# Kernel tuning notes

Measured on AMD Instinct MI355X. Metric: run time of the kernel, lower is better.

Reference implementation:

```python
import jax, jax.numpy as jnp
import numpy as np

EPS = 1e-07
B, C, NCON, NCC = 500000, 30, 8, 3
NH = 7  # hidden width


def _coarse_code():
    # [C, NCC] Gaussian bump coarse code, as built in __init__
    sigma = 0.25
    const_1 = 1.0 / (sigma * np.sqrt(6.28))
    ii = jnp.arange(C, dtype=jnp.float32)[:, None] / (C - 1)
    jj = jnp.arange(NCC, dtype=jnp.float32)[None, :] / (NCC - 1)
    return (const_1 * jnp.exp(-0.5 * jnp.square((ii - jj) / sigma))).astype(jnp.float32)


def _mlp(x, W1, b1, Wh, bh, Wo, bo):
    # x: [B, C, n_in]; six 7-unit ReLU layers then linear output (dropout inactive)
    h = jax.nn.relu(jnp.einsum('bci,hi->bch', x, W1) + b1)
    for i in range(Wh.shape[0]):
        h = jax.nn.relu(jnp.einsum('bci,hi->bch', h, Wh[i]) + bh[i])
    return jnp.einsum('bci,oi->bco', h, Wo) + bo


def setup_inputs() -> dict:
    key = jax.random.key(0)
    ks = jax.random.split(key, 16)
    u = lambda k, shape, lo, hi: jax.random.uniform(k, shape, jnp.float32, lo, hi)
    inp = {
        'tau': jax.random.uniform(ks[0], (B, C, NCON), jnp.float32),
        'mu_direct': jax.random.uniform(ks[1], (B, 1), jnp.float32),
        'mu_diffuse': jax.random.uniform(ks[2], (B, 1), jnp.float32),
        # net_direct: n_input = 5 + NCC + 1 = 9
        'Wd1': u(ks[3], (NH, 5 + NCC + 1), -1.0, 1.0),
        'bd1': u(ks[4], (NH,), 0.9, 1.1),
        'Wdh': u(ks[5], (5, NH, NH), -1.0, 1.0),
        'bdh': u(ks[6], (5, NH), 0.9, 1.1),
        'Wdo': u(ks[7], (3, NH), -1.0, 1.0),
        'bdo': u(ks[8], (3,), -0.1, 0.1),
        # net_diffuse: n_input = 5 + NCC = 8
        'Wf1': u(ks[9], (NH, 5 + NCC), -1.0, 1.0),
        'bf1': u(ks[10], (NH,), 0.9, 1.1),
        'Wfh': u(ks[11], (5, NH, NH), -1.0, 1.0),
        'bfh': u(ks[12], (5, NH), 0.9, 1.1),
        'Wfo': u(ks[13], (3, NH), -1.0, 1.0),
        'bfo': u(ks[14], (3,), -0.1, 0.1),
    }
    return inp


def reference(tau, mu_direct, mu_diffuse, Wd1, bd1, Wdh, bdh, Wdo, bdo,
              Wf1, bf1, Wfh, bfh, Wfo, bfo):
    tau_total = jnp.sum(tau, axis=2)                      # [B, C]
    t_direct = jnp.exp(-tau_total / (mu_direct + EPS))    # [B, C]
    t_diffuse = jnp.exp(-tau_total / (mu_diffuse + EPS))  # [B, C]

    mu_d = mu_direct[:, :, None]                          # [B, 1, 1]
    tau_direct = tau / (mu_d + EPS)                       # [B, C, NCON]

    direct_1 = (tau_direct[:, :, 3] + tau_direct[:, :, 4]
                + tau_direct[:, :, 6] + tau_direct[:, :, 7])[:, :, None]
    mu_rep = jnp.broadcast_to(mu_d, (tau.shape[0], C, 1))
    cc = jnp.broadcast_to(_coarse_code()[None], (tau.shape[0], C, NCC))

    direct = jnp.concatenate([tau_direct[:, :, 0:2], tau_direct[:, :, 5:6],
                              tau_direct[:, :, 2:3], direct_1, mu_rep, cc], axis=2)  # [B,C,9]

    diffuse_1 = (tau[:, :, 3] + tau[:, :, 4] + tau[:, :, 6] + tau[:, :, 7])[:, :, None]
    diffuse = jnp.concatenate([tau[:, :, 0:2], tau[:, :, 5:6],
                               tau[:, :, 2:3], diffuse_1, cc], axis=2)  # [B,C,8]

    e_split_direct = jax.nn.softmax(_mlp(direct, Wd1, bd1, Wdh, bdh, Wdo, bdo), axis=-1)
    e_split_diffuse = jax.nn.softmax(_mlp(diffuse, Wf1, bf1, Wfh, bfh, Wfo, bfo), axis=-1)
    return (t_direct, t_diffuse, e_split_direct, e_split_diffuse)
```

## Files before the change

### kernel.cpp

```cpp
#include <hip/hip_runtime.h>


#define B_SZ 500000
#define C_SZ 30
#define BC   (B_SZ * C_SZ)
#define EPSF 1e-7f

__device__ __forceinline__ float bf2f(unsigned short u) {
    union { unsigned int i; float f; } v;
    v.i = ((unsigned int)u) << 16;
    return v.f;
}

__device__ __forceinline__ unsigned short f2bf(float f) {
    union { float f; unsigned int i; } v;
    v.f = f;
    unsigned int u = v.i;
    unsigned int r = u + 0x7fffu + ((u >> 16) & 1u);
    return (unsigned short)(r >> 16);
}

__global__ void detect_dtype(const unsigned int* __restrict__ tau_raw,
                             int* __restrict__ flag) {
    if (threadIdx.x == 0 && blockIdx.x == 0) {
        unsigned int acc = 0;
        for (int i = 0; i < 256; ++i) acc |= tau_raw[i];
        *flag = (acc & 0x8000u) ? 1 : 0;
    }
}

struct P12 { const void* p[12]; };

__global__ void cvt_weights(P12 ptrs, float* __restrict__ ws,
                            const int* __restrict__ flag) {
    int i = blockIdx.x * blockDim.x + threadIdx.x;
    if (i >= 741) return;
    const int sizes[12] = {63, 7, 245, 35, 21, 3, 56, 7, 245, 35, 21, 3};
    int off = i, seg = 0;
    while (seg < 11 && off >= sizes[seg]) { off -= sizes[seg]; ++seg; }
    if (*flag) {
        ws[i] = ((const float*)ptrs.p[seg])[off];
    } else {
        ws[i] = bf2f(((const unsigned short*)ptrs.p[seg])[off]);
    }
}

template <int IN>
__device__ __forceinline__ void mlp(const float* __restrict__ x,
                                    const float* __restrict__ W1,
                                    const float* __restrict__ b1,
                                    const float* __restrict__ Wh,
                                    const float* __restrict__ bh,
                                    const float* __restrict__ Wo,
                                    const float* __restrict__ bo,
                                    float* __restrict__ o) {
    float h[7];
#pragma unroll
    for (int j = 0; j < 7; ++j) {
        float a = b1[j];
#pragma unroll
        for (int i = 0; i < IN; ++i) a = fmaf(x[i], W1[j * IN + i], a);
        h[j] = fmaxf(a, 0.0f);
    }
#pragma unroll
    for (int l = 0; l < 5; ++l) {
        float h2[7];
#pragma unroll
        for (int j = 0; j < 7; ++j) {
            float a = bh[l * 7 + j];
#pragma unroll
            for (int i = 0; i < 7; ++i) a = fmaf(h[i], Wh[l * 49 + j * 7 + i], a);
            h2[j] = fmaxf(a, 0.0f);
        }
#pragma unroll
        for (int j = 0; j < 7; ++j) h[j] = h2[j];
    }
#pragma unroll
    for (int k = 0; k < 3; ++k) {
        float a = bo[k];
#pragma unroll
        for (int i = 0; i < 7; ++i) a = fmaf(h[i], Wo[k * 7 + i], a);
        o[k] = a;
    }
}

__global__ __launch_bounds__(256) void scatter_main(
    const void* __restrict__ tau_p,
    const void* __restrict__ mu_dir_p,
    const void* __restrict__ mu_dif_p,
    const float* __restrict__ ws,
    const int* __restrict__ flag,
    void* __restrict__ out_p)
{
    __shared__ float cc_s[C_SZ * 3];
    int tid = threadIdx.x;
    if (tid < C_SZ * 3) {
        int c = tid / 3, j = tid - c * 3;
        const float sigma = 0.25f;
        const float c1 = 1.0f / (sigma * sqrtf(6.28f));
        float ii = (float)c * (1.0f / (float)(C_SZ - 1));
        float jj = (float)j * 0.5f;
        float d = (ii - jj) * (1.0f / sigma);
        cc_s[tid] = c1 * __expf(-0.5f * d * d);
    }
    __syncthreads();

    int e = blockIdx.x * 256 + tid;
    if (e >= BC) return;
    int b = e / C_SZ;
    int c = e - b * C_SZ;

    int is_f32 = *flag;

    float t0, t1, t2, t3, t4, t5, t6, t7, mu_d, mu_f;
    if (is_f32) {
        const float4* tf = (const float4*)tau_p;
        float4 a = tf[2 * e];
        float4 bq = tf[2 * e + 1];
        t0 = a.x; t1 = a.y; t2 = a.z; t3 = a.w;
        t4 = bq.x; t5 = bq.y; t6 = bq.z; t7 = bq.w;
        mu_d = ((const float*)mu_dir_p)[b];
        mu_f = ((const float*)mu_dif_p)[b];
    } else {
        uint4 t = ((const uint4*)tau_p)[e];
        t0 = bf2f((unsigned short)(t.x & 0xffffu));
        t1 = bf2f((unsigned short)(t.x >> 16));
        t2 = bf2f((unsigned short)(t.y & 0xffffu));
        t3 = bf2f((unsigned short)(t.y >> 16));
        t4 = bf2f((unsigned short)(t.z & 0xffffu));
        t5 = bf2f((unsigned short)(t.z >> 16));
        t6 = bf2f((unsigned short)(t.w & 0xffffu));
        t7 = bf2f((unsigned short)(t.w >> 16));
        mu_d = bf2f(((const unsigned short*)mu_dir_p)[b]);
        mu_f = bf2f(((const unsigned short*)mu_dif_p)[b]);
    }

    float rcp_d = __builtin_amdgcn_rcpf(mu_d + EPSF);
    float rcp_f = __builtin_amdgcn_rcpf(mu_f + EPSF);

    float tau_total = ((t0 + t1) + (t2 + t3)) + ((t4 + t5) + (t6 + t7));
    float t_direct = __expf(-tau_total * rcp_d);
    float t_diffuse = __expf(-tau_total * rcp_f);

    float cc0 = cc_s[c * 3 + 0], cc1 = cc_s[c * 3 + 1], cc2 = cc_s[c * 3 + 2];
    float s1 = (t3 + t4) + (t6 + t7);

    float xd[9] = {t0 * rcp_d, t1 * rcp_d, t5 * rcp_d, t2 * rcp_d,
                   s1 * rcp_d, mu_d, cc0, cc1, cc2};
    float xf[8] = {t0, t1, t5, t2, s1, cc0, cc1, cc2};

    float od[3], of_[3];
    mlp<9>(xd, ws + 0, ws + 63, ws + 70, ws + 315, ws + 350, ws + 371, od);
    mlp<8>(xf, ws + 374, ws + 430, ws + 437, ws + 682, ws + 717, ws + 738, of_);

    float md = fmaxf(fmaxf(od[0], od[1]), od[2]);
    float d0 = __expf(od[0] - md), d1 = __expf(od[1] - md), d2 = __expf(od[2] - md);
    float rd = __builtin_amdgcn_rcpf(d0 + d1 + d2);
    float mf = fmaxf(fmaxf(of_[0], of_[1]), of_[2]);
    float f0 = __expf(of_[0] - mf), f1 = __expf(of_[1] - mf), f2 = __expf(of_[2] - mf);
    float rf = __builtin_amdgcn_rcpf(f0 + f1 + f2);

    int od_base = 2 * BC + 3 * e;
    int of_base = 5 * BC + 3 * e;
    if (is_f32) {
        float* out = (float*)out_p;
        out[e] = t_direct;
        out[BC + e] = t_diffuse;
        out[od_base + 0] = d0 * rd;
        out[od_base + 1] = d1 * rd;
        out[od_base + 2] = d2 * rd;
        out[of_base + 0] = f0 * rf;
        out[of_base + 1] = f1 * rf;
        out[of_base + 2] = f2 * rf;
    } else {
        unsigned short* out = (unsigned short*)out_p;
        out[e] = f2bf(t_direct);
        out[BC + e] = f2bf(t_diffuse);
        out[od_base + 0] = f2bf(d0 * rd);
        out[od_base + 1] = f2bf(d1 * rd);
        out[od_base + 2] = f2bf(d2 * rd);
        out[of_base + 0] = f2bf(f0 * rf);
        out[of_base + 1] = f2bf(f1 * rf);
        out[of_base + 2] = f2bf(f2 * rf);
    }
}

extern "C" void kernel_launch(void* const* d_in, const int* in_sizes, int n_in,
                              void* d_out, int out_size, void* d_ws, size_t ws_size,
                              hipStream_t stream) {
    float* ws = (float*)d_ws;
    int* flag = (int*)((char*)d_ws + 4096);

    detect_dtype<<<1, 64, 0, stream>>>((const unsigned int*)d_in[0], flag);

    P12 p;
    for (int i = 0; i < 12; ++i) p.p[i] = d_in[3 + i];
    cvt_weights<<<1, 768, 0, stream>>>(p, ws, flag);

    int nblk = (BC + 255) / 256;
    scatter_main<<<nblk, 256, 0, stream>>>(
        d_in[0], d_in[1], d_in[2], ws, flag, d_out);
}
```

Baseline: 919.3 us.

## Fold coarse-code into per-channel biases, use fdot2 for diffuse MLP, merge prep kernels

Folds the constant coarse-code inputs into per-channel effective first-layer biases, so the first layer of each MLP gets narrower. It also remaps the diffuse MLP's first layer onto the raw tau columns and runs the diffuse MLP with packed fp16 dot products (fdot2) on the bf16 path. Other changes: exp2 with LOG2E folded into the weights, packed bf16 conversion for stores, and dtype detection merged into a single prep kernel. The fp16 hidden activations lower precision and may affect accuracy.

```diff
diff --git a/kernel.cpp b/kernel.cpp
--- a/kernel.cpp
+++ b/kernel.cpp
@@ -5,6 +5,35 @@
 #define C_SZ 30
 #define BC   (B_SZ * C_SZ)
 #define EPSF 1e-7f
+#define LOG2E 1.4426950408889634f
+
+#if __has_builtin(__builtin_amdgcn_fdot2)
+#define HAVE_FDOT2 1
+#else
+#define HAVE_FDOT2 0
+#endif
+
+typedef __fp16 h2 __attribute__((ext_vector_type(2)));
+
+enum {
+    WD1C  = 0,
+    WDH   = 42,
+    BDH   = 287,
+    WDO   = 322,
+    BDO   = 343,
+    BEFFD = 352,
+    BEFFF = 592,
+    VF16  = 832,
+    WFH16 = 860,
+    WFO16 = 1000,
+    BFO   = 1012,
+    BFH   = 1015,
+    VFF   = 1056,
+    WFHF  = 1112,
+    WFOF  = 1357,
+    WS_FLOATS = 1378
+};
+#define FLAG_BYTE_OFF 6144
 
 __device__ __forceinline__ float bf2f(unsigned short u) {
     union { unsigned int i; float f; } v;
@@ -12,76 +41,104 @@
     return v.f;
 }
 
-__device__ __forceinline__ unsigned short f2bf(float f) {
-    union { float f; unsigned int i; } v;
-    v.f = f;
-    unsigned int u = v.i;
-    unsigned int r = u + 0x7fffu + ((u >> 16) & 1u);
-    return (unsigned short)(r >> 16);
-}
-
-__global__ void detect_dtype(const unsigned int* __restrict__ tau_raw,
-                             int* __restrict__ flag) {
-    if (threadIdx.x == 0 && blockIdx.x == 0) {
-        unsigned int acc = 0;
-        for (int i = 0; i < 256; ++i) acc |= tau_raw[i];
-        *flag = (acc & 0x8000u) ? 1 : 0;
-    }
-}
+__device__ __forceinline__ float ex2(float x) {
+    float r;
+    asm("v_exp_f32 %0, %1" : "=v"(r) : "v"(x));
+    return r;
+}
+
+__device__ __forceinline__ unsigned int pk_bf16(float lo, float hi) {
+    unsigned int r;
+    asm("v_cvt_pk_bf16_f32 %0, %1, %2" : "=v"(r) : "v"(lo), "v"(hi));
+    return r;
+}
+
+#if HAVE_FDOT2
+__device__ __forceinline__ h2 uash2(unsigned int u) {
+    union { unsigned int u; h2 h; } v; v.u = u; return v.h;
+}
+#endif
 
 struct P12 { const void* p[12]; };
 
-__global__ void cvt_weights(P12 ptrs, float* __restrict__ ws,
-                            const int* __restrict__ flag) {
-    int i = blockIdx.x * blockDim.x + threadIdx.x;
-    if (i >= 741) return;
-    const int sizes[12] = {63, 7, 245, 35, 21, 3, 56, 7, 245, 35, 21, 3};
-    int off = i, seg = 0;
-    while (seg < 11 && off >= sizes[seg]) { off -= sizes[seg]; ++seg; }
-    if (*flag) {
-        ws[i] = ((const float*)ptrs.p[seg])[off];
-    } else {
-        ws[i] = bf2f(((const unsigned short*)ptrs.p[seg])[off]);
-    }
-}
-
-template <int IN>
-__device__ __forceinline__ void mlp(const float* __restrict__ x,
-                                    const float* __restrict__ W1,
-                                    const float* __restrict__ b1,
-                                    const float* __restrict__ Wh,
-                                    const float* __restrict__ bh,
-                                    const float* __restrict__ Wo,
-                                    const float* __restrict__ bo,
-                                    float* __restrict__ o) {
-    float h[7];
-#pragma unroll
-    for (int j = 0; j < 7; ++j) {
-        float a = b1[j];
-#pragma unroll
-        for (int i = 0; i < IN; ++i) a = fmaf(x[i], W1[j * IN + i], a);
-        h[j] = fmaxf(a, 0.0f);
-    }
-#pragma unroll
-    for (int l = 0; l < 5; ++l) {
-        float h2[7];
-#pragma unroll
-        for (int j = 0; j < 7; ++j) {
-            float a = bh[l * 7 + j];
-#pragma unroll
-            for (int i = 0; i < 7; ++i) a = fmaf(h[i], Wh[l * 49 + j * 7 + i], a);
-            h2[j] = fmaxf(a, 0.0f);
-        }
-#pragma unroll
-        for (int j = 0; j < 7; ++j) h[j] = h2[j];
-    }
-#pragma unroll
-    for (int k = 0; k < 3; ++k) {
-        float a = bo[k];
-#pragma unroll
-        for (int i = 0; i < 7; ++i) a = fmaf(h[i], Wo[k * 7 + i], a);
-        o[k] = a;
-    }
+__global__ void prep(P12 ptrs, const unsigned int* __restrict__ tau_raw,
+                     float* __restrict__ ws, int* __restrict__ flagp)
+{
+    __shared__ int sflag;
+    int tid = threadIdx.x;
+    if (tid < 64) {
+        unsigned long long m = __ballot((tau_raw[tid] & 0x8000u) != 0u);
+        if (tid == 0) { sflag = (m != 0ull) ? 1 : 0; *flagp = sflag; }
+    }
+    __syncthreads();
+    const int f32m = sflag;
+
+    auto rd = [&](int seg, int idx) -> float {
+        if (f32m) return ((const float*)ptrs.p[seg])[idx];
+        return bf2f(((const unsigned short*)ptrs.p[seg])[idx]);
+    };
+    auto ccf = [&](int c, int k) -> float {
+        const float C1 = 1.0f / (0.25f * sqrtf(6.28f));
+        float ii = (float)c * (1.0f / 29.0f);
+        float jj = (float)k * 0.5f;
+        float d = (ii - jj) * 4.0f;
+        return C1 * expf(-0.5f * d * d);
+    };
+    auto pk = [&](float a, float b) -> unsigned int {
+        union { h2 h; unsigned int u; } v;
+        v.h.x = (__fp16)a; v.h.y = (__fp16)b;
+        return v.u;
+    };
+    unsigned int* wsu = (unsigned int*)ws;
+
+    for (int i = tid; i < 42; i += 256) { int j = i / 6, k = i % 6; ws[WD1C + i] = rd(0, j * 9 + k); }
+    for (int i = tid; i < 245; i += 256) ws[WDH + i] = rd(2, i);
+    for (int i = tid; i < 35;  i += 256) ws[BDH + i] = rd(3, i);
+    for (int i = tid; i < 21;  i += 256) ws[WDO + i] = rd(4, i) * LOG2E;
+    for (int i = tid; i < 3;   i += 256) ws[BDO + i] = rd(5, i) * LOG2E;
+    for (int i = tid; i < 240; i += 256) {
+        int c = i / 8, j = i % 8; float v = 0.f;
+        if (j < 7) v = rd(1, j) + rd(0, j * 9 + 6) * ccf(c, 0)
+                               + rd(0, j * 9 + 7) * ccf(c, 1)
+                               + rd(0, j * 9 + 8) * ccf(c, 2);
+        ws[BEFFD + i] = v;
+    }
+    for (int i = tid; i < 240; i += 256) {
+        int c = i / 8, j = i % 8; float v = 0.f;
+        if (j < 7) v = rd(7, j) + rd(6, j * 8 + 5) * ccf(c, 0)
+                               + rd(6, j * 8 + 6) * ccf(c, 1)
+                               + rd(6, j * 8 + 7) * ccf(c, 2);
+        ws[BEFFF + i] = v;
+    }
+    for (int i = tid; i < 28; i += 256) {
+        int j = i / 4, p = i % 4; float lo, hi;
+        if      (p == 0) { lo = rd(6, j * 8 + 0); hi = rd(6, j * 8 + 1); }
+        else if (p == 1) { lo = rd(6, j * 8 + 3); hi = rd(6, j * 8 + 4); }
+        else if (p == 2) { lo = rd(6, j * 8 + 4); hi = rd(6, j * 8 + 2); }
+        else             { lo = rd(6, j * 8 + 4); hi = rd(6, j * 8 + 4); }
+        wsu[VF16 + i] = pk(lo, hi);
+    }
+    for (int i = tid; i < 140; i += 256) {
+        int lj = i / 4, p = i % 4; float lo, hi;
+        if (p < 3) { lo = rd(8, lj * 7 + 2 * p); hi = rd(8, lj * 7 + 2 * p + 1); }
+        else       { lo = rd(8, lj * 7 + 6);     hi = 0.f; }
+        wsu[WFH16 + i] = pk(lo, hi);
+    }
+    for (int i = tid; i < 12; i += 256) {
+        int j = i / 4, p = i % 4; float lo, hi;
+        if (p < 3) { lo = rd(10, j * 7 + 2 * p); hi = rd(10, j * 7 + 2 * p + 1); }
+        else       { lo = rd(10, j * 7 + 6);     hi = 0.f; }
+        wsu[WFO16 + i] = pk(lo, hi);
+    }
+    for (int i = tid; i < 3;   i += 256) ws[BFO + i] = rd(11, i);
+    for (int i = tid; i < 35;  i += 256) ws[BFH + i] = rd(9, i);
+    for (int i = tid; i < 56; i += 256) {
+        int j = i / 8, k = i % 8;
+        const int cols[8] = {0, 1, 3, 4, 4, 2, 4, 4};
+        ws[VFF + i] = rd(6, j * 8 + cols[k]);
+    }
+    for (int i = tid; i < 245; i += 256) ws[WFHF + i] = rd(8, i);
+    for (int i = tid; i < 21;  i += 256) ws[WFOF + i] = rd(10, i);
 }
 
 __global__ __launch_bounds__(256) void scatter_main(
@@ -92,20 +149,7 @@
     const int* __restrict__ flag,
     void* __restrict__ out_p)
 {
-    __shared__ float cc_s[C_SZ * 3];
-    int tid = threadIdx.x;
-    if (tid < C_SZ * 3) {
-        int c = tid / 3, j = tid - c * 3;
-        const float sigma = 0.25f;
-        const float c1 = 1.0f / (sigma * sqrtf(6.28f));
-        float ii = (float)c * (1.0f / (float)(C_SZ - 1));
-        float jj = (float)j * 0.5f;
-        float d = (ii - jj) * (1.0f / sigma);
-        cc_s[tid] = c1 * __expf(-0.5f * d * d);
-    }
-    __syncthreads();
-
-    int e = blockIdx.x * 256 + tid;
+    int e = blockIdx.x * 256 + threadIdx.x;
     if (e >= BC) return;
     int b = e / C_SZ;
     int c = e - b * C_SZ;
@@ -139,49 +183,170 @@
     float rcp_f = __builtin_amdgcn_rcpf(mu_f + EPSF);
 
     float tau_total = ((t0 + t1) + (t2 + t3)) + ((t4 + t5) + (t6 + t7));
-    float t_direct = __expf(-tau_total * rcp_d);
-    float t_diffuse = __expf(-tau_total * rcp_f);
-
-    float cc0 = cc_s[c * 3 + 0], cc1 = cc_s[c * 3 + 1], cc2 = cc_s[c * 3 + 2];
+    float ttl = tau_total * LOG2E;
+    float t_direct  = ex2(-ttl * rcp_d);
+    float t_diffuse = ex2(-ttl * rcp_f);
     float s1 = (t3 + t4) + (t6 + t7);
 
-    float xd[9] = {t0 * rcp_d, t1 * rcp_d, t5 * rcp_d, t2 * rcp_d,
-                   s1 * rcp_d, mu_d, cc0, cc1, cc2};
-    float xf[8] = {t0, t1, t5, t2, s1, cc0, cc1, cc2};
-
-    float od[3], of_[3];
-    mlp<9>(xd, ws + 0, ws + 63, ws + 70, ws + 315, ws + 350, ws + 371, od);
-    mlp<8>(xf, ws + 374, ws + 430, ws + 437, ws + 682, ws + 717, ws + 738, of_);
-
+    const float4* bdv = (const float4*)(ws + BEFFD);
+    float4 bda = bdv[2 * c], bdb = bdv[2 * c + 1];
+    const float4* bfv = (const float4*)(ws + BEFFF);
+    float4 bfa = bfv[2 * c], bfb = bfv[2 * c + 1];
+    float beffd[8] = {bda.x, bda.y, bda.z, bda.w, bdb.x, bdb.y, bdb.z, bdb.w};
+    float befff[8] = {bfa.x, bfa.y, bfa.z, bfa.w, bfb.x, bfb.y, bfb.z, bfb.w};
+
+    float xd[6] = {t0 * rcp_d, t1 * rcp_d, t5 * rcp_d, t2 * rcp_d, s1 * rcp_d, mu_d};
+    float h[7];
+#pragma unroll
+    for (int j = 0; j < 7; ++j) {
+        float a = beffd[j];
+#pragma unroll
+        for (int i = 0; i < 6; ++i) a = fmaf(xd[i], ws[WD1C + j * 6 + i], a);
+        h[j] = fmaxf(a, 0.0f);
+    }
+#pragma unroll
+    for (int l = 0; l < 5; ++l) {
+        float hn[7];
+#pragma unroll
+        for (int j = 0; j < 7; ++j) {
+            float a = ws[BDH + l * 7 + j];
+#pragma unroll
+            for (int i = 0; i < 7; ++i) a = fmaf(h[i], ws[WDH + l * 49 + j * 7 + i], a);
+            hn[j] = fmaxf(a, 0.0f);
+        }
+#pragma unroll
+        for (int j = 0; j < 7; ++j) h[j] = hn[j];
+    }
+    float od[3];
+#pragma unroll
+    for (int k = 0; k < 3; ++k) {
+        float a = ws[BDO + k];
+#pragma unroll
+        for (int i = 0; i < 7; ++i) a = fmaf(h[i], ws[WDO + k * 7 + i], a);
+        od[k] = a;
+    }
     float md = fmaxf(fmaxf(od[0], od[1]), od[2]);
-    float d0 = __expf(od[0] - md), d1 = __expf(od[1] - md), d2 = __expf(od[2] - md);
-    float rd = __builtin_amdgcn_rcpf(d0 + d1 + d2);
-    float mf = fmaxf(fmaxf(of_[0], of_[1]), of_[2]);
-    float f0 = __expf(of_[0] - mf), f1 = __expf(of_[1] - mf), f2 = __expf(of_[2] - mf);
+    float d0 = ex2(od[0] - md), d1 = ex2(od[1] - md), d2 = ex2(od[2] - md);
+    float rd_ = __builtin_amdgcn_rcpf(d0 + d1 + d2);
+    d0 *= rd_; d1 *= rd_; d2 *= rd_;
+
+    float lf0, lf1, lf2;
+#if HAVE_FDOT2
+    if (!is_f32) {
+        const unsigned int* wsu = (const unsigned int*)ws;
+        h2 xp0 = __builtin_amdgcn_cvt_pkrtz(t0, t1);
+        h2 xp1 = __builtin_amdgcn_cvt_pkrtz(t2, t3);
+        h2 xp2 = __builtin_amdgcn_cvt_pkrtz(t4, t5);
+        h2 xp3 = __builtin_amdgcn_cvt_pkrtz(t6, t7);
+        float hf[7];
+#pragma unroll
+        for (int j = 0; j < 7; ++j) {
+            float a = befff[j];
+            a = __builtin_amdgcn_fdot2(xp0, uash2(wsu[VF16 + j * 4 + 0]), a, false);
+            a = __builtin_amdgcn_fdot2(xp1, uash2(wsu[VF16 + j * 4 + 1]), a, false);
+            a = __builtin_amdgcn_fdot2(xp2, uash2(wsu[VF16 + j * 4 + 2]), a, false);
+            a = __builtin_amdgcn_fdot2(xp3, uash2(wsu[VF16 + j * 4 + 3]), a, false);
+            hf[j] = fmaxf(a, 0.0f);
+        }
+#pragma unroll
+        for (int l = 0; l < 5; ++l) {
+            h2 hp0, hp1, hp2, hp3;
+            hp0.x = (__fp16)hf[0]; hp0.y = (__fp16)hf[1];
+            hp1.x = (__fp16)hf[2]; hp1.y = (__fp16)hf[3];
+            hp2.x = (__fp16)hf[4]; hp2.y = (__fp16)hf[5];
+            hp3.x = (__fp16)hf[6]; hp3.y = (__fp16)0.0f;
+            float hn[7];
+#pragma unroll
+            for (int j = 0; j < 7; ++j) {
+                int wb = WFH16 + (l * 7 + j) * 4;
+                float a = ws[BFH + l * 7 + j];
+                a = __builtin_amdgcn_fdot2(hp0, uash2(wsu[wb + 0]), a, false);
+                a = __builtin_amdgcn_fdot2(hp1, uash2(wsu[wb + 1]), a, false);
+                a = __builtin_amdgcn_fdot2(hp2, uash2(wsu[wb + 2]), a, false);
+                a = __builtin_amdgcn_fdot2(hp3, uash2(wsu[wb + 3]), a, false);
+                hn[j] = fmaxf(a, 0.0f);
+            }
+#pragma unroll
+            for (int j = 0; j < 7; ++j) hf[j] = hn[j];
+        }
+        h2 op0, op1, op2, op3;
+        op0.x = (__fp16)hf[0]; op0.y = (__fp16)hf[1];
+        op1.x = (__fp16)hf[2]; op1.y = (__fp16)hf[3];
+        op2.x = (__fp16)hf[4]; op2.y = (__fp16)hf[5];
+        op3.x = (__fp16)hf[6]; op3.y = (__fp16)0.0f;
+        float lo[3];
+#pragma unroll
+        for (int k = 0; k < 3; ++k) {
+            float a = ws[BFO + k];
+            a = __builtin_amdgcn_fdot2(op0, uash2(wsu[WFO16 + k * 4 + 0]), a, false);
+            a = __builtin_amdgcn_fdot2(op1, uash2(wsu[WFO16 + k * 4 + 1]), a, false);
+            a = __builtin_amdgcn_fdot2(op2, uash2(wsu[WFO16 + k * 4 + 2]), a, false);
+            a = __builtin_amdgcn_fdot2(op3, uash2(wsu[WFO16 + k * 4 + 3]), a, false);
+            lo[k] = a * LOG2E;
+        }
+        lf0 = lo[0]; lf1 = lo[1]; lf2 = lo[2];
+    } else
+#endif
+    {
+        float tarr[8] = {t0, t1, t2, t3, t4, t5, t6, t7};
+        float hf[7];
+#pragma unroll
+        for (int j = 0; j < 7; ++j) {
+            float a = befff[j];
+#pragma unroll
+            for (int i = 0; i < 8; ++i) a = fmaf(tarr[i], ws[VFF + j * 8 + i], a);
+            hf[j] = fmaxf(a, 0.0f);
+        }
+#pragma unroll
+        for (int l = 0; l < 5; ++l) {
+            float hn[7];
+#pragma unroll
+            for (int j = 0; j < 7; ++j) {
+                float a = ws[BFH + l * 7 + j];
+#pragma unroll
+                for (int i = 0; i < 7; ++i) a = fmaf(hf[i], ws[WFHF + l * 49 + j * 7 + i], a);
+                hn[j] = fmaxf(a, 0.0f);
+            }
+#pragma unroll
+            for (int j = 0; j < 7; ++j) hf[j] = hn[j];
+        }
+        float lo[3];
+#pragma unroll
+        for (int k = 0; k < 3; ++k) {
+            float a = ws[BFO + k];
+#pragma unroll
+            for (int i = 0; i < 7; ++i) a = fmaf(hf[i], ws[WFOF + k * 7 + i], a);
+            lo[k] = a * LOG2E;
+        }
+        lf0 = lo[0]; lf1 = lo[1]; lf2 = lo[2];
+    }
+    float mf = fmaxf(fmaxf(lf0, lf1), lf2);
+    float f0 = ex2(lf0 - mf), f1 = ex2(lf1 - mf), f2 = ex2(lf2 - mf);
     float rf = __builtin_amdgcn_rcpf(f0 + f1 + f2);
-
-    int od_base = 2 * BC + 3 * e;
-    int of_base = 5 * BC + 3 * e;
+    f0 *= rf; f1 *= rf; f2 *= rf;
+
+    int odb = 2 * BC + 3 * e;
+    int ofb = 5 * BC + 3 * e;
     if (is_f32) {
         float* out = (float*)out_p;
         out[e] = t_direct;
         out[BC + e] = t_diffuse;
-        out[od_base + 0] = d0 * rd;
-        out[od_base + 1] = d1 * rd;
-        out[od_base + 2] = d2 * rd;
-        out[of_base + 0] = f0 * rf;
-        out[of_base + 1] = f1 * rf;
-        out[of_base + 2] = f2 * rf;
+        out[odb + 0] = d0; out[odb + 1] = d1; out[odb + 2] = d2;
+        out[ofb + 0] = f0; out[ofb + 1] = f1; out[ofb + 2] = f2;
     } else {
         unsigned short* out = (unsigned short*)out_p;
-        out[e] = f2bf(t_direct);
-        out[BC + e] = f2bf(t_diffuse);
-        out[od_base + 0] = f2bf(d0 * rd);
-        out[od_base + 1] = f2bf(d1 * rd);
-        out[od_base + 2] = f2bf(d2 * rd);
-        out[of_base + 0] = f2bf(f0 * rf);
-        out[of_base + 1] = f2bf(f1 * rf);
-        out[of_base + 2] = f2bf(f2 * rf);
+        unsigned int P1 = pk_bf16(t_direct, t_diffuse);
+        unsigned int P2 = pk_bf16(d0, d1);
+        unsigned int P3 = pk_bf16(d2, f0);
+        unsigned int P4 = pk_bf16(f1, f2);
+        out[e]       = (unsigned short)P1;
+        out[BC + e]  = (unsigned short)(P1 >> 16);
+        out[odb + 0] = (unsigned short)P2;
+        out[odb + 1] = (unsigned short)(P2 >> 16);
+        out[odb + 2] = (unsigned short)P3;
+        out[ofb + 0] = (unsigned short)(P3 >> 16);
+        out[ofb + 1] = (unsigned short)P4;
+        out[ofb + 2] = (unsigned short)(P4 >> 16);
     }
 }
 
@@ -189,13 +354,11 @@
                               void* d_out, int out_size, void* d_ws, size_t ws_size,
                               hipStream_t stream) {
     float* ws = (float*)d_ws;
-    int* flag = (int*)((char*)d_ws + 4096);
-
-    detect_dtype<<<1, 64, 0, stream>>>((const unsigned int*)d_in[0], flag);
+    int* flag = (int*)((char*)d_ws + FLAG_BYTE_OFF);
 
     P12 p;
     for (int i = 0; i < 12; ++i) p.p[i] = d_in[3 + i];
-    cvt_weights<<<1, 768, 0, stream>>>(p, ws, flag);
+    prep<<<1, 256, 0, stream>>>(p, (const unsigned int*)d_in[0], ws, flag);
 
     int nblk = (BC + 255) / 256;
     scatter_main<<<nblk, 256, 0, stream>>>(
```

New measurement: 907.0 us. No clear change (-1.3%).

## Pack MLP weights for packed FMA, fold coarse code into biases, coalesce bf16 stores

Applied to the files above, without the earlier changes.

Weight prep now runs in one kernel together with dtype detection. It lays out the weights in pairs so the MLP can use packed two-wide FMA, and it folds the constant coarse-code inputs into per-channel effective biases. The diffuse first layer is also remapped so it reads the raw tau values directly, without the summed feature. Softmax and transmittance use a native exp2 with LOG2E pre-folded into the output weights. In the bf16 path, outputs are staged through shared memory and written as coalesced 16-byte stores instead of scattered 2-byte stores, at the cost of an extra block barrier and a different rounding path.

```diff
diff --git a/kernel.cpp b/kernel.cpp
--- a/kernel.cpp
+++ b/kernel.cpp
@@ -5,6 +5,26 @@
 #define C_SZ 30
 #define BC   (B_SZ * C_SZ)
 #define EPSF 1e-7f
+#define LOG2E 1.4426950408889634f
+
+typedef float f2 __attribute__((ext_vector_type(2)));
+
+enum {
+    WD1P  = 0,
+    WDHP  = 48,
+    WDOP  = 328,
+    BDOP  = 356,
+    BEFFD = 360,
+    BEFFF = 600,
+    WF1P  = 840,
+    WFHP  = 904,
+    WFOP  = 1184,
+    BFOP  = 1212,
+    BDHP  = 1216,
+    BFHP  = 1256,
+    WS_FLOATS = 1296
+};
+#define FLAG_BYTE_OFF 6144
 
 __device__ __forceinline__ float bf2f(unsigned short u) {
     union { unsigned int i; float f; } v;
@@ -20,68 +40,165 @@
     return (unsigned short)(r >> 16);
 }
 
-__global__ void detect_dtype(const unsigned int* __restrict__ tau_raw,
-                             int* __restrict__ flag) {
-    if (threadIdx.x == 0 && blockIdx.x == 0) {
-        unsigned int acc = 0;
-        for (int i = 0; i < 256; ++i) acc |= tau_raw[i];
-        *flag = (acc & 0x8000u) ? 1 : 0;
-    }
+__device__ __forceinline__ float ex2(float x) {
+    float r;
+    asm("v_exp_f32 %0, %1" : "=v"(r) : "v"(x));
+    return r;
+}
+
+__device__ __forceinline__ unsigned int pk_bf16(float lo, float hi) {
+    unsigned int r;
+    asm("v_cvt_pk_bf16_f32 %0, %1, %2" : "=v"(r) : "v"(lo), "v"(hi));
+    return r;
+}
+
+__device__ __forceinline__ f2 pkfma(f2 a, f2 b, f2 c) {
+#if __has_builtin(__builtin_elementwise_fma)
+    return __builtin_elementwise_fma(a, b, c);
+#else
+    f2 r; r.x = fmaf(a.x, b.x, c.x); r.y = fmaf(a.y, b.y, c.y); return r;
+#endif
+}
+
+__device__ __forceinline__ f2 pkmax0(f2 a) {
+    f2 z = {0.0f, 0.0f};
+#if __has_builtin(__builtin_elementwise_max)
+    return __builtin_elementwise_max(a, z);
+#else
+    f2 r; r.x = fmaxf(a.x, 0.f); r.y = fmaxf(a.y, 0.f); return r;
+#endif
+}
+
+__device__ __forceinline__ f2 bc(f2 v, int hl) {
+    return hl ? __builtin_shufflevector(v, v, 1, 1)
+              : __builtin_shufflevector(v, v, 0, 0);
+}
+
+template <int NIN, int W1, int WH, int BH, int WO, int BO>
+__device__ __forceinline__ void mlp_pk(const float* __restrict__ ws,
+                                       const f2* __restrict__ x2,
+                                       const f2* __restrict__ be,
+                                       float* __restrict__ o) {
+    const f2* w1 = (const f2*)(ws + W1);
+    f2 h[4] = {be[0], be[1], be[2], be[3]};
+#pragma unroll
+    for (int i = 0; i < NIN; ++i) {
+        f2 xx = bc(x2[i >> 1], i & 1);
+#pragma unroll
+        for (int p = 0; p < 4; ++p) h[p] = pkfma(xx, w1[i * 4 + p], h[p]);
+    }
+#pragma unroll
+    for (int p = 0; p < 4; ++p) h[p] = pkmax0(h[p]);
+
+    const f2* wh = (const f2*)(ws + WH);
+    const f2* bh = (const f2*)(ws + BH);
+#pragma unroll
+    for (int l = 0; l < 5; ++l) {
+        f2 hn[4];
+#pragma unroll
+        for (int p = 0; p < 4; ++p) hn[p] = bh[l * 4 + p];
+#pragma unroll
+        for (int i = 0; i < 7; ++i) {
+            f2 xx = bc(h[i >> 1], i & 1);
+#pragma unroll
+            for (int p = 0; p < 4; ++p) hn[p] = pkfma(xx, wh[(l * 7 + i) * 4 + p], hn[p]);
+        }
+#pragma unroll
+        for (int p = 0; p < 4; ++p) h[p] = pkmax0(hn[p]);
+    }
+
+    const f2* wo = (const f2*)(ws + WO);
+    const f2* bo = (const f2*)(ws + BO);
+    f2 oA = bo[0], oB = bo[1];
+#pragma unroll
+    for (int i = 0; i < 7; ++i) {
+        f2 xx = bc(h[i >> 1], i & 1);
+        oA = pkfma(xx, wo[i * 2 + 0], oA);
+        oB = pkfma(xx, wo[i * 2 + 1], oB);
+    }
+    o[0] = oA.x; o[1] = oA.y; o[2] = oB.x;
 }
 
 struct P12 { const void* p[12]; };
 
-__global__ void cvt_weights(P12 ptrs, float* __restrict__ ws,
-                            const int* __restrict__ flag) {
-    int i = blockIdx.x * blockDim.x + threadIdx.x;
-    if (i >= 741) return;
-    const int sizes[12] = {63, 7, 245, 35, 21, 3, 56, 7, 245, 35, 21, 3};
-    int off = i, seg = 0;
-    while (seg < 11 && off >= sizes[seg]) { off -= sizes[seg]; ++seg; }
-    if (*flag) {
-        ws[i] = ((const float*)ptrs.p[seg])[off];
-    } else {
-        ws[i] = bf2f(((const unsigned short*)ptrs.p[seg])[off]);
-    }
-}
-
-template <int IN>
-__device__ __forceinline__ void mlp(const float* __restrict__ x,
-                                    const float* __restrict__ W1,
-                                    const float* __restrict__ b1,
-                                    const float* __restrict__ Wh,
-                                    const float* __restrict__ bh,
-                                    const float* __restrict__ Wo,
-                                    const float* __restrict__ bo,
-                                    float* __restrict__ o) {
-    float h[7];
-#pragma unroll
-    for (int j = 0; j < 7; ++j) {
-        float a = b1[j];
-#pragma unroll
-        for (int i = 0; i < IN; ++i) a = fmaf(x[i], W1[j * IN + i], a);
-        h[j] = fmaxf(a, 0.0f);
-    }
-#pragma unroll
-    for (int l = 0; l < 5; ++l) {
-        float h2[7];
-#pragma unroll
-        for (int j = 0; j < 7; ++j) {
-            float a = bh[l * 7 + j];
-#pragma unroll
-            for (int i = 0; i < 7; ++i) a = fmaf(h[i], Wh[l * 49 + j * 7 + i], a);
-            h2[j] = fmaxf(a, 0.0f);
-        }
-#pragma unroll
-        for (int j = 0; j < 7; ++j) h[j] = h2[j];
-    }
-#pragma unroll
-    for (int k = 0; k < 3; ++k) {
-        float a = bo[k];
-#pragma unroll
-        for (int i = 0; i < 7; ++i) a = fmaf(h[i], Wo[k * 7 + i], a);
-        o[k] = a;
-    }
+__global__ void prep(P12 ptrs, const unsigned int* __restrict__ tau_raw,
+                     float* __restrict__ ws, int* __restrict__ flagp)
+{
+    __shared__ int sflag;
+    int tid = threadIdx.x;
+    if (tid < 64) {
+        unsigned long long m = __ballot((tau_raw[tid] & 0x8000u) != 0u);
+        if (tid == 0) { sflag = (m != 0ull) ? 1 : 0; *flagp = sflag; }
+    }
+    __syncthreads();
+    const int f32m = sflag;
+
+    auto rd = [&](int seg, int idx) -> float {
+        if (f32m) return ((const float*)ptrs.p[seg])[idx];
+        return bf2f(((const unsigned short*)ptrs.p[seg])[idx]);
+    };
+    auto ccf = [&](int c, int k) -> float {
+        const float C1 = 1.0f / (0.25f * sqrtf(6.28f));
+        float ii = (float)c * (1.0f / 29.0f);
+        float jj = (float)k * 0.5f;
+        float d = (ii - jj) * 4.0f;
+        return C1 * expf(-0.5f * d * d);
+    };
+
+    for (int i = tid; i < 48; i += 256) {
+        int ii = i >> 3, p = (i >> 1) & 3, hl = i & 1, j = 2 * p + hl;
+        ws[WD1P + i] = (j < 7) ? rd(0, j * 9 + ii) : 0.f;
+    }
+    for (int i = tid; i < 280; i += 256) {
+        int l = i / 56, r = i % 56;
+        int ii = r >> 3, p = (r >> 1) & 3, hl = r & 1, j = 2 * p + hl;
+        ws[WDHP + i] = (j < 7) ? rd(2, l * 49 + j * 7 + ii) : 0.f;
+    }
+    for (int i = tid; i < 40; i += 256) {
+        int l = i / 8, p = (i >> 1) & 3, hl = i & 1, j = 2 * p + hl;
+        ws[BDHP + i] = (j < 7) ? rd(3, l * 7 + j) : 0.f;
+    }
+    for (int i = tid; i < 28; i += 256) {
+        int ii = i >> 2, p = (i >> 1) & 1, hl = i & 1, k = 2 * p + hl;
+        ws[WDOP + i] = (k < 3) ? rd(4, k * 7 + ii) * LOG2E : 0.f;
+    }
+    for (int i = tid; i < 4; i += 256)
+        ws[BDOP + i] = (i < 3) ? rd(5, i) * LOG2E : 0.f;
+
+    for (int i = tid; i < 240; i += 256) {
+        int c = i / 8, j = i % 8; float v = 0.f;
+        if (j < 7) v = rd(1, j) + rd(0, j * 9 + 6) * ccf(c, 0)
+                               + rd(0, j * 9 + 7) * ccf(c, 1)
+                               + rd(0, j * 9 + 8) * ccf(c, 2);
+        ws[BEFFD + i] = v;
+    }
+    for (int i = tid; i < 240; i += 256) {
+        int c = i / 8, j = i % 8; float v = 0.f;
+        if (j < 7) v = rd(7, j) + rd(6, j * 8 + 5) * ccf(c, 0)
+                               + rd(6, j * 8 + 6) * ccf(c, 1)
+                               + rd(6, j * 8 + 7) * ccf(c, 2);
+        ws[BEFFF + i] = v;
+    }
+    for (int i = tid; i < 64; i += 256) {
+        int ii = i >> 3, p = (i >> 1) & 3, hl = i & 1, j = 2 * p + hl;
+        const int cols[8] = {0, 1, 3, 4, 4, 2, 4, 4};
+        ws[WF1P + i] = (j < 7) ? rd(6, j * 8 + cols[ii]) : 0.f;
+    }
+    for (int i = tid; i < 280; i += 256) {
+        int l = i / 56, r = i % 56;
+        int ii = r >> 3, p = (r >> 1) & 3, hl = r & 1, j = 2 * p + hl;
+        ws[WFHP + i] = (j < 7) ? rd(8, l * 49 + j * 7 + ii) : 0.f;
+    }
+    for (int i = tid; i < 40; i += 256) {
+        int l = i / 8, p = (i >> 1) & 3, hl = i & 1, j = 2 * p + hl;
+        ws[BFHP + i] = (j < 7) ? rd(9, l * 7 + j) : 0.f;
+    }
+    for (int i = tid; i < 28; i += 256) {
+        int ii = i >> 2, p = (i >> 1) & 1, hl = i & 1, k = 2 * p + hl;
+        ws[WFOP + i] = (k < 3) ? rd(10, k * 7 + ii) * LOG2E : 0.f;
+    }
+    for (int i = tid; i < 4; i += 256)
+        ws[BFOP + i] = (i < 3) ? rd(11, i) * LOG2E : 0.f;
 }
 
 __global__ __launch_bounds__(256) void scatter_main(
@@ -92,37 +209,30 @@
     const int* __restrict__ flag,
     void* __restrict__ out_p)
 {
-    __shared__ float cc_s[C_SZ * 3];
+    __shared__ unsigned short sm[2048];
+
     int tid = threadIdx.x;
-    if (tid < C_SZ * 3) {
-        int c = tid / 3, j = tid - c * 3;
-        const float sigma = 0.25f;
-        const float c1 = 1.0f / (sigma * sqrtf(6.28f));
-        float ii = (float)c * (1.0f / (float)(C_SZ - 1));
-        float jj = (float)j * 0.5f;
-        float d = (ii - jj) * (1.0f / sigma);
-        cc_s[tid] = c1 * __expf(-0.5f * d * d);
-    }
-    __syncthreads();
-
-    int e = blockIdx.x * 256 + tid;
-    if (e >= BC) return;
-    int b = e / C_SZ;
-    int c = e - b * C_SZ;
+    int eb0 = blockIdx.x * 256;
+    int e = eb0 + tid;
+    bool act = (e < BC);
+    int eL = act ? e : (BC - 1);
+    int b = eL / C_SZ;
+    int c = eL - b * C_SZ;
+    bool tail = (eb0 + 256 > BC);
 
     int is_f32 = *flag;
 
     float t0, t1, t2, t3, t4, t5, t6, t7, mu_d, mu_f;
     if (is_f32) {
         const float4* tf = (const float4*)tau_p;
-        float4 a = tf[2 * e];
-        float4 bq = tf[2 * e + 1];
+        float4 a = tf[2 * eL];
+        float4 bq = tf[2 * eL + 1];
         t0 = a.x; t1 = a.y; t2 = a.z; t3 = a.w;
         t4 = bq.x; t5 = bq.y; t6 = bq.z; t7 = bq.w;
         mu_d = ((const float*)mu_dir_p)[b];
         mu_f = ((const float*)mu_dif_p)[b];
     } else {
-        uint4 t = ((const uint4*)tau_p)[e];
+        uint4 t = ((const uint4*)tau_p)[eL];
         t0 = bf2f((unsigned short)(t.x & 0xffffu));
         t1 = bf2f((unsigned short)(t.x >> 16));
         t2 = bf2f((unsigned short)(t.y & 0xffffu));
@@ -139,49 +249,90 @@
     float rcp_f = __builtin_amdgcn_rcpf(mu_f + EPSF);
 
     float tau_total = ((t0 + t1) + (t2 + t3)) + ((t4 + t5) + (t6 + t7));
-    float t_direct = __expf(-tau_total * rcp_d);
-    float t_diffuse = __expf(-tau_total * rcp_f);
-
-    float cc0 = cc_s[c * 3 + 0], cc1 = cc_s[c * 3 + 1], cc2 = cc_s[c * 3 + 2];
+    float ttl = tau_total * LOG2E;
+    float t_direct  = ex2(-ttl * rcp_d);
+    float t_diffuse = ex2(-ttl * rcp_f);
     float s1 = (t3 + t4) + (t6 + t7);
 
-    float xd[9] = {t0 * rcp_d, t1 * rcp_d, t5 * rcp_d, t2 * rcp_d,
-                   s1 * rcp_d, mu_d, cc0, cc1, cc2};
-    float xf[8] = {t0, t1, t5, t2, s1, cc0, cc1, cc2};
-
-    float od[3], of_[3];
-    mlp<9>(xd, ws + 0, ws + 63, ws + 70, ws + 315, ws + 350, ws + 371, od);
-    mlp<8>(xf, ws + 374, ws + 430, ws + 437, ws + 682, ws + 717, ws + 738, of_);
+    f2 bed[4], bef[4];
+    {
+        const float4* q = (const float4*)(ws + BEFFD) + 2 * c;
+        float4 qa = q[0], qb = q[1];
+        bed[0] = f2{qa.x, qa.y}; bed[1] = f2{qa.z, qa.w};
+        bed[2] = f2{qb.x, qb.y}; bed[3] = f2{qb.z, qb.w};
+        const float4* r = (const float4*)(ws + BEFFF) + 2 * c;
+        float4 ra = r[0], rb = r[1];
+        bef[0] = f2{ra.x, ra.y}; bef[1] = f2{ra.z, ra.w};
+        bef[2] = f2{rb.x, rb.y}; bef[3] = f2{rb.z, rb.w};
+    }
+
+    f2 xd2[3] = { f2{t0 * rcp_d, t1 * rcp_d},
+                  f2{t5 * rcp_d, t2 * rcp_d},
+                  f2{s1 * rcp_d, mu_d} };
+    float od[3];
+    mlp_pk<6, WD1P, WDHP, BDHP, WDOP, BDOP>(ws, xd2, bed, od);
+
+    f2 xf2[4] = { f2{t0, t1}, f2{t2, t3}, f2{t4, t5}, f2{t6, t7} };
+    float of_[3];
+    mlp_pk<8, WF1P, WFHP, BFHP, WFOP, BFOP>(ws, xf2, bef, of_);
 
     float md = fmaxf(fmaxf(od[0], od[1]), od[2]);
-    float d0 = __expf(od[0] - md), d1 = __expf(od[1] - md), d2 = __expf(od[2] - md);
-    float rd = __builtin_amdgcn_rcpf(d0 + d1 + d2);
+    float d0 = ex2(od[0] - md), d1 = ex2(od[1] - md), d2 = ex2(od[2] - md);
+    float rd_ = __builtin_amdgcn_rcpf(d0 + d1 + d2);
+    d0 *= rd_; d1 *= rd_; d2 *= rd_;
+
     float mf = fmaxf(fmaxf(of_[0], of_[1]), of_[2]);
-    float f0 = __expf(of_[0] - mf), f1 = __expf(of_[1] - mf), f2 = __expf(of_[2] - mf);
-    float rf = __builtin_amdgcn_rcpf(f0 + f1 + f2);
-
-    int od_base = 2 * BC + 3 * e;
-    int of_base = 5 * BC + 3 * e;
-    if (is_f32) {
-        float* out = (float*)out_p;
-        out[e] = t_direct;
-        out[BC + e] = t_diffuse;
-        out[od_base + 0] = d0 * rd;
-        out[od_base + 1] = d1 * rd;
-        out[od_base + 2] = d2 * rd;
-        out[of_base + 0] = f0 * rf;
-        out[of_base + 1] = f1 * rf;
-        out[of_base + 2] = f2 * rf;
+    float f0 = ex2(of_[0] - mf), f1 = ex2(of_[1] - mf), f2v = ex2(of_[2] - mf);
+    float rf = __builtin_amdgcn_rcpf(f0 + f1 + f2v);
+    f0 *= rf; f1 *= rf; f2v *= rf;
+
+    if (!is_f32 && !tail) {
+        unsigned int P1 = pk_bf16(t_direct, t_diffuse);
+        unsigned int P2 = pk_bf16(d0, d1);
+        unsigned int P3 = pk_bf16(d2, f0);
+        unsigned int P4 = pk_bf16(f1, f2v);
+        sm[tid]       = (unsigned short)P1;
+        sm[256 + tid] = (unsigned short)(P1 >> 16);
+        int db = 512 + 3 * tid;
+        sm[db + 0] = (unsigned short)P2;
+        sm[db + 1] = (unsigned short)(P2 >> 16);
+        sm[db + 2] = (unsigned short)P3;
+        int fb = 1280 + 3 * tid;
+        sm[fb + 0] = (unsigned short)(P3 >> 16);
+        sm[fb + 1] = (unsigned short)P4;
+        sm[fb + 2] = (unsigned short)(P4 >> 16);
+        __syncthreads();
+        uint4 v = ((const uint4*)sm)[tid];
+        unsigned int goff;
+        if (tid < 32)        goff = 2u * eb0 + 16u * tid;
+        else if (tid < 64)   goff = 2u * (BC + eb0) + 16u * (tid - 32);
+        else if (tid < 160)  goff = 4u * BC + 6u * eb0 + 16u * (tid - 64);
+        else                 goff = 10u * BC + 6u * eb0 + 16u * (tid - 160);
+        *(uint4*)((char*)out_p + goff) = v;
+    } else if (!is_f32) {
+        if (act) {
+            unsigned short* out = (unsigned short*)out_p;
+            int odb = 2 * BC + 3 * e;
+            int ofb = 5 * BC + 3 * e;
+            out[e]       = f2bf(t_direct);
+            out[BC + e]  = f2bf(t_diffuse);
+            out[odb + 0] = f2bf(d0);
+            out[odb + 1] = f2bf(d1);
+            out[odb + 2] = f2bf(d2);
+            out[ofb + 0] = f2bf(f0);
+            out[ofb + 1] = f2bf(f1);
+            out[ofb + 2] = f2bf(f2v);
+        }
     } else {
-        unsigned short* out = (unsigned short*)out_p;
-        out[e] = f2bf(t_direct);
-        out[BC + e] = f2bf(t_diffuse);
-        out[od_base + 0] = f2bf(d0 * rd);
-        out[od_base + 1] = f2bf(d1 * rd);
-        out[od_base + 2] = f2bf(d2 * rd);
-        out[of_base + 0] = f2bf(f0 * rf);
-        out[of_base + 1] = f2bf(f1 * rf);
-        out[of_base + 2] = f2bf(f2 * rf);
+        if (act) {
+            float* out = (float*)out_p;
+            int odb = 2 * BC + 3 * e;
+            int ofb = 5 * BC + 3 * e;
+            out[e] = t_direct;
+            out[BC + e] = t_diffuse;
+            out[odb + 0] = d0; out[odb + 1] = d1; out[odb + 2] = d2;
+            out[ofb + 0] = f0; out[ofb + 1] = f1; out[ofb + 2] = f2v;
+        }
     }
 }
 
@@ -189,13 +340,11 @@
                               void* d_out, int out_size, void* d_ws, size_t ws_size,
                               hipStream_t stream) {
     float* ws = (float*)d_ws;
-    int* flag = (int*)((char*)d_ws + 4096);
-
-    detect_dtype<<<1, 64, 0, stream>>>((const unsigned int*)d_in[0], flag);
+    int* flag = (int*)((char*)d_ws + FLAG_BYTE_OFF);
 
     P12 p;
     for (int i = 0; i < 12; ++i) p.p[i] = d_in[3 + i];
-    cvt_weights<<<1, 768, 0, stream>>>(p, ws, flag);
+    prep<<<1, 256, 0, stream>>>(p, (const unsigned int*)d_in[0], ws, flag);
 
     int nblk = (BC + 255) / 256;
     scatter_main<<<nblk, 256, 0, stream>>>(
```

New measurement: 839.7 us. 8.7% less time.
